# Kernel tuning notes

Measured on AMD Instinct MI355X. Metric: run time of the kernel, lower is better.

## Reference

```python
import jax, jax.numpy as jnp
import numpy as np

SPATIAL = ((100, 100), (50, 50), (25, 25), (13, 13))
STARTS = [0]
for _h, _w in SPATIAL[:-1]:
    STARTS.append(STARTS[-1] + _h * _w)
L_TOTAL = sum(h * w for h, w in SPATIAL)  # 13294
D, DFFN, NL, NH, NP = 256, 1024, 4, 8, 4
DH = D // NH
EPS = 1e-5


def _ln(x, g, b):
    mu = x.mean(-1, keepdims=True)
    var = ((x - mu) ** 2).mean(-1, keepdims=True)
    return (x - mu) * jax.lax.rsqrt(var + EPS) * g + b


def _bilinear(v_l, x, y, H, W):
    # v_l: [B,NH,H*W,DH]; x,y: [B,NH,Q*NP] pixel coords (grid_sample align_corners=False, zero padding)
    x0f = jnp.floor(x); y0f = jnp.floor(y)
    lx, ly = x - x0f, y - y0f
    x0 = x0f.astype(jnp.int32); y0 = y0f.astype(jnp.int32)
    acc = 0.0
    for dx, dy, w in ((0, 0, (1 - lx) * (1 - ly)), (1, 0, lx * (1 - ly)),
                      (0, 1, (1 - lx) * ly), (1, 1, lx * ly)):
        xi, yi = x0 + dx, y0 + dy
        valid = (xi >= 0) & (xi < W) & (yi >= 0) & (yi < H)
        idx = jnp.clip(yi, 0, H - 1) * W + jnp.clip(xi, 0, W - 1)
        g = jnp.take_along_axis(v_l, idx[..., None], axis=2)  # [B,NH,Q*NP,DH]
        acc = acc + g * (w * valid.astype(w.dtype))[..., None]
    return acc


def _msdeform(query, value_in, ref, norm_wh, Woff, boff, Wattn, battn, Wval, bval, Wout, bout):
    B, Q, _ = query.shape
    v = (value_in @ Wval + bval).reshape(B, L_TOTAL, NH, DH)
    off = (query @ Woff + boff).reshape(B, Q, NH, NL, NP, 2)
    aw = (query @ Wattn + battn).reshape(B, Q, NH, NL * NP)
    aw = jax.nn.softmax(aw, axis=-1).reshape(B, Q, NH, NL, NP)
    # normalized sampling locations in [0,1]: ref + offset / (W,H)
    loc = ref[:, :, None, :, None, :] + off / norm_wh[None, None, None, :, None, :]
    out = 0.0
    for l, (H, W) in enumerate(SPATIAL):
        s = STARTS[l]
        v_l = v[:, s:s + H * W].transpose(0, 2, 1, 3)          # [B,NH,HW,DH]
        loc_l = loc[:, :, :, l].transpose(0, 2, 1, 3, 4)       # [B,NH,Q,NP,2]
        x = (loc_l[..., 0] * W - 0.5).reshape(B, NH, Q * NP)
        y = (loc_l[..., 1] * H - 0.5).reshape(B, NH, Q * NP)
        samp = _bilinear(v_l, x, y, H, W).reshape(B, NH, Q, NP, DH)
        w_l = aw[:, :, :, l].transpose(0, 2, 1, 3)             # [B,NH,Q,NP]
        out = out + (samp * w_l[..., None]).sum(3)             # [B,NH,Q,DH]
    out = out.transpose(0, 2, 1, 3).reshape(B, Q, D)
    return out @ Wout + bout


def setup_inputs() -> dict:
    key = jax.random.key(0)
    ks = jax.random.split(key, 12)
    B = 4
    s = 0.02
    return {
        "src": jax.random.normal(ks[0], (B, L_TOTAL, D), jnp.float32),
        "pos": jax.random.normal(ks[1], (B, L_TOTAL, D), jnp.float32),
        "reference_points": jax.random.uniform(ks[2], (B, L_TOTAL, NL, 2), jnp.float32),
        "spatial_shapes": jnp.array(SPATIAL, jnp.int32),
        "level_start_index": jnp.array(STARTS, jnp.int32),
        "W_off": jax.random.normal(ks[3], (D, NH * NL * NP * 2), jnp.float32) * 0.01,
        "b_off": jax.random.normal(ks[4], (NH * NL * NP * 2,), jnp.float32) * 0.5,
        "W_attn": jax.random.normal(ks[5], (D, NH * NL * NP), jnp.float32) * s,
        "b_attn": jnp.zeros((NH * NL * NP,), jnp.float32),
        "W_val": jax.random.normal(ks[6], (D, D), jnp.float32) * s,
        "b_val": jnp.zeros((D,), jnp.float32),
        "W_out": jax.random.normal(ks[7], (D, D), jnp.float32) * s,
        "b_out": jnp.zeros((D,), jnp.float32),
        "ln_sa_g": jnp.ones((D,), jnp.float32),
        "ln_sa_b": jnp.zeros((D,), jnp.float32),
        "W1": jax.random.normal(ks[8], (D, DFFN), jnp.float32) * s,
        "b1": jnp.zeros((DFFN,), jnp.float32),
        "W2": jax.random.normal(ks[9], (DFFN, D), jnp.float32) * s,
        "b2": jnp.zeros((D,), jnp.float32),
        "ln_ff_g": jnp.ones((D,), jnp.float32),
        "ln_ff_b": jnp.zeros((D,), jnp.float32),
    }


def reference(src, pos, reference_points, spatial_shapes, level_start_index,
              W_off, b_off, W_attn, b_attn, W_val, b_val, W_out, b_out,
              ln_sa_g, ln_sa_b, W1, b1, W2, b2, ln_ff_g, ln_ff_b):
    # offset normalizer is (W, H) per level
    norm_wh = jnp.stack([spatial_shapes[:, 1], spatial_shapes[:, 0]], -1).astype(src.dtype)
    q = src + pos  # with_pos_embed
    sa = _msdeform(q, src, reference_points, norm_wh,
                   W_off, b_off, W_attn, b_attn, W_val, b_val, W_out, b_out)
    x = _ln(sa + src, ln_sa_g, ln_sa_b)          # dropout = identity (eval)
    y = jnp.maximum(x @ W1 + b1, 0.0) @ W2 + b2  # relu FFN
    return _ln(y + x, ln_ff_g, ln_ff_b)
```

## Files before the change

kernel.cpp:

```cpp
#include <hip/hip_runtime.h>
#include <hip/hip_bf16.h>

typedef __hip_bfloat16 bf16;
typedef short bf16x8 __attribute__((ext_vector_type(8)));
typedef float f32x4  __attribute__((ext_vector_type(4)));

#define ROWS 53176
#define LTOT 13294

__device__ __forceinline__ float b2f(bf16 v) { return __bfloat162float(v); }

__device__ __forceinline__ void gl2lds16(const void* g, void* l) {
    __builtin_amdgcn_global_load_lds(
        (const __attribute__((address_space(1))) unsigned*)g,
        (__attribute__((address_space(3))) unsigned*)l, 16, 0, 0);
}

template<bool RELU>
__global__ __launch_bounds__(256, 2)
void gemm_bs_n(const bf16* __restrict__ A, const bf16* __restrict__ Bt,
               const float* __restrict__ bias, bf16* __restrict__ C,
               int M, int N)
{
    __shared__ __align__(16) char Bsb[65536];
    const int tid  = threadIdx.x;
    const int wave = tid >> 6, lane = tid & 63;
    const int l15 = lane & 15, quad = lane >> 4;
    const int swz = (lane & 7) << 4;
    const int m0 = blockIdx.y * 256, n0 = blockIdx.x * 128;

    const char* Btb = (const char*)(Bt + (size_t)n0 * 256);
#pragma unroll
    for (int it = 0; it < 16; ++it) {
        int c = it * 256 + tid;
        int srcoff = (c * 16) ^ (((c >> 5) & 7) << 4);
        gl2lds16(Btb + srcoff, Bsb + (it * 256 + wave * 64) * 16);
    }

    const bf16* aptr[4];
#pragma unroll
    for (int i = 0; i < 4; ++i) {
        int r = m0 + wave * 64 + i * 16 + l15;
        if (r > M - 1) r = M - 1;
        aptr[i] = A + (size_t)r * 256;
    }

    f32x4 acc[4][8];
#pragma unroll
    for (int i = 0; i < 4; ++i)
#pragma unroll
        for (int j = 0; j < 8; ++j) acc[i][j] = (f32x4){0.f, 0.f, 0.f, 0.f};

    __syncthreads();

#pragma unroll
    for (int kc = 0; kc < 8; ++kc) {
        bf16x8 af[4], bfr[8];
#pragma unroll
        for (int i = 0; i < 4; ++i)
            af[i] = *(const bf16x8*)(aptr[i] + kc * 32 + quad * 8);
#pragma unroll
        for (int j = 0; j < 8; ++j) {
            int boff = ((j * 16 + l15) * 512 + kc * 64 + quad * 16) ^ swz;
            bfr[j] = *(const bf16x8*)&Bsb[boff];
        }
#pragma unroll
        for (int i = 0; i < 4; ++i)
#pragma unroll
            for (int j = 0; j < 8; ++j)
                acc[i][j] = __builtin_amdgcn_mfma_f32_16x16x32_bf16(bfr[j], af[i], acc[i][j], 0, 0, 0);
    }

    float4 b4[8];
#pragma unroll
    for (int j = 0; j < 8; ++j)
        b4[j] = *(const float4*)&bias[n0 + j * 16 + quad * 4];

#pragma unroll
    for (int i = 0; i < 4; ++i) {
        int gm = m0 + wave * 64 + i * 16 + l15;
        if (gm >= M) continue;
#pragma unroll
        for (int j = 0; j < 8; ++j) {
            int gn = n0 + j * 16 + quad * 4;
            union { bf16 h[4]; uint2 u2; } pk;
#pragma unroll
            for (int r = 0; r < 4; ++r) {
                float v = acc[i][j][r] + ((const float*)&b4[j])[r];
                if (RELU) v = fmaxf(v, 0.f);
                pk.h[r] = __float2bfloat16(v);
            }
            *(uint2*)&C[(size_t)gm * N + gn] = pk.u2;
        }
    }
}

template<typename OT, int K>
__global__ __launch_bounds__(256, 2)
void gemm_bs_ln(const bf16* __restrict__ A, const bf16* __restrict__ Bt,
                const float* __restrict__ bias, const bf16* __restrict__ res,
                OT* __restrict__ C, const float* __restrict__ gam,
                const float* __restrict__ bet, int M)
{
    __shared__ __align__(16) char Bsb[65536];
    const int tid  = threadIdx.x;
    const int wave = tid >> 6, lane = tid & 63;
    const int l15 = lane & 15, quad = lane >> 4;
    const int swz = (lane & 7) << 4;
    const int m0 = blockIdx.x * 128;

    const bf16* aptr[2];
#pragma unroll
    for (int i = 0; i < 2; ++i) {
        int r = m0 + wave * 32 + i * 16 + l15;
        if (r > M - 1) r = M - 1;
        aptr[i] = A + (size_t)r * K;
    }

    f32x4 acc[2][16];
#pragma unroll
    for (int i = 0; i < 2; ++i)
#pragma unroll
        for (int j = 0; j < 16; ++j) acc[i][j] = (f32x4){0.f, 0.f, 0.f, 0.f};

    for (int kc = 0; kc < K / 128; ++kc) {
#pragma unroll
        for (int it = 0; it < 16; ++it) {
            int c = it * 256 + tid;
            int row = c >> 4, col = c & 15;
            size_t srcoff = (size_t)row * (K * 2) + kc * 256
                          + ((col * 16) ^ ((row & 7) << 4));
            gl2lds16((const char*)Bt + srcoff, Bsb + (it * 256 + wave * 64) * 16);
        }
        __syncthreads();
#pragma unroll
        for (int t = 0; t < 4; ++t) {
            bf16x8 af[2], bfr[16];
#pragma unroll
            for (int i = 0; i < 2; ++i)
                af[i] = *(const bf16x8*)(aptr[i] + kc * 128 + t * 32 + quad * 8);
#pragma unroll
            for (int j = 0; j < 16; ++j) {
                int boff = ((j * 16 + l15) * 256 + t * 64 + quad * 16) ^ swz;
                bfr[j] = *(const bf16x8*)&Bsb[boff];
            }
#pragma unroll
            for (int i = 0; i < 2; ++i)
#pragma unroll
                for (int j = 0; j < 16; ++j)
                    acc[i][j] = __builtin_amdgcn_mfma_f32_16x16x32_bf16(bfr[j], af[i], acc[i][j], 0, 0, 0);
        }
        __syncthreads();
    }

#pragma unroll
    for (int i = 0; i < 2; ++i) {
        int gm = m0 + wave * 32 + i * 16 + l15;
        bool valid = gm < M;
        float lsum = 0.f, lsq = 0.f;
#pragma unroll
        for (int j = 0; j < 16; ++j) {
            int gn = j * 16 + quad * 4;
            float4 b4 = *(const float4*)&bias[gn];
            float r4[4] = {0.f, 0.f, 0.f, 0.f};
            if (valid) {
                uint2 ru = *(const uint2*)&res[(size_t)gm * 256 + gn];
                const bf16* rh = (const bf16*)&ru;
#pragma unroll
                for (int r = 0; r < 4; ++r) r4[r] = b2f(rh[r]);
            }
#pragma unroll
            for (int r = 0; r < 4; ++r) {
                float v = acc[i][j][r] + ((const float*)&b4)[r] + r4[r];
                acc[i][j][r] = v;
                lsum += v;
                lsq  += v * v;
            }
        }
#pragma unroll
        for (int mask = 16; mask <= 32; mask <<= 1) {
            lsum += __shfl_xor(lsum, mask);
            lsq  += __shfl_xor(lsq, mask);
        }
        if (!valid) continue;
        float mean = lsum * (1.f / 256.f);
        float var  = lsq * (1.f / 256.f) - mean * mean;
        float rstd = rsqrtf(fmaxf(var, 0.f) + 1e-5f);
#pragma unroll
        for (int j = 0; j < 16; ++j) {
            int gn = j * 16 + quad * 4;
            float4 g4  = *(const float4*)&gam[gn];
            float4 be4 = *(const float4*)&bet[gn];
            if constexpr (sizeof(OT) == 2) {
                union { bf16 h[4]; uint2 u2; } pk;
#pragma unroll
                for (int r = 0; r < 4; ++r)
                    pk.h[r] = __float2bfloat16((acc[i][j][r] - mean) * rstd *
                              ((const float*)&g4)[r] + ((const float*)&be4)[r]);
                *(uint2*)&((bf16*)C)[(size_t)gm * 256 + gn] = pk.u2;
            } else {
                float4 o;
#pragma unroll
                for (int r = 0; r < 4; ++r)
                    ((float*)&o)[r] = (acc[i][j][r] - mean) * rstd *
                              ((const float*)&g4)[r] + ((const float*)&be4)[r];
                *(float4*)&((float*)C)[(size_t)gm * 256 + gn] = o;
            }
        }
    }
}

__global__ void cast_qs_kernel(const float* __restrict__ s, const float* __restrict__ p,
                               bf16* __restrict__ sb, bf16* __restrict__ qb, int n4)
{
    int i = blockIdx.x * 256 + threadIdx.x;
    if (i >= n4) return;
    float4 sv = ((const float4*)s)[i];
    float4 pv = ((const float4*)p)[i];
    union { bf16 h[4]; uint2 u; } a, b;
    a.h[0] = __float2bfloat16(sv.x); a.h[1] = __float2bfloat16(sv.y);
    a.h[2] = __float2bfloat16(sv.z); a.h[3] = __float2bfloat16(sv.w);
    b.h[0] = __float2bfloat16(sv.x + pv.x); b.h[1] = __float2bfloat16(sv.y + pv.y);
    b.h[2] = __float2bfloat16(sv.z + pv.z); b.h[3] = __float2bfloat16(sv.w + pv.w);
    ((uint2*)sb)[i] = a.u;
    ((uint2*)qb)[i] = b.u;
}

__global__ void wcast_all(const float* __restrict__ Wval, const float* __restrict__ Woff,
                          const float* __restrict__ Wattn, const float* __restrict__ Wout,
                          const float* __restrict__ W1, const float* __restrict__ W2,
                          const float* __restrict__ boff, const float* __restrict__ battn,
                          bf16* __restrict__ Wval_t, bf16* __restrict__ Wcat_t,
                          bf16* __restrict__ Wout_t, bf16* __restrict__ W1_t,
                          bf16* __restrict__ W2_t, float* __restrict__ bcat)
{
    int e = blockIdx.x * 256 + threadIdx.x;
    if (e < 384) bcat[e] = (e < 256) ? boff[e] : battn[e - 256];
    if (e < 65536) {
        int n = e >> 8, k = e & 255;
        Wval_t[e] = __float2bfloat16(Wval[k * 256 + n]);
    } else if (e < 163840) {
        int i = e - 65536; int n = i >> 8, k = i & 255;
        float w = (n < 256) ? Woff[k * 256 + n] : Wattn[k * 128 + (n - 256)];
        Wcat_t[i] = __float2bfloat16(w);
    } else if (e < 229376) {
        int i = e - 163840; int n = i >> 8, k = i & 255;
        Wout_t[i] = __float2bfloat16(Wout[k * 256 + n]);
    } else if (e < 491520) {
        int i = e - 229376; int n = i >> 8, k = i & 255;
        W1_t[i] = __float2bfloat16(W1[k * 1024 + n]);
    } else if (e < 753664) {
        int i = e - 491520; int n = i >> 10, k = i & 1023;
        W2_t[i] = __float2bfloat16(W2[k * 256 + n]);
    }
}

__global__ __launch_bounds__(256)
void sample_kernel(const bf16* __restrict__ v, const bf16* __restrict__ ocat,
                   const float* __restrict__ ref, bf16* __restrict__ samp)
{
    __shared__ int4 tab[16][33];
    const int tid = threadIdx.x;
    const int grp = tid >> 4, lane = tid & 15;
    const int gidx = blockIdx.x * 16 + grp;
    const int h = gidx & 7, bq = gidx >> 3, b = bq / LTOT;

    {
        const int p = lane, l = p >> 2, pp = p & 3;
        const int W = (l == 0) ? 100 : (l == 1) ? 50 : (l == 2) ? 25 : 13;
        const int S = (l == 0) ? 0 : (l == 1) ? 10000 : (l == 2) ? 12500 : 13125;
        const float fW = (float)W;
        float rx = ref[(size_t)bq * 8 + l * 2 + 0];
        float ry = ref[(size_t)bq * 8 + l * 2 + 1];
        const bf16* ob = ocat + (size_t)bq * 384;
        float ox = b2f(ob[h * 32 + l * 8 + pp * 2 + 0]);
        float oy = b2f(ob[h * 32 + l * 8 + pp * 2 + 1]);
        float lg = b2f(ob[256 + h * 16 + p]);
        float m = lg;
#pragma unroll
        for (int mask = 1; mask <= 8; mask <<= 1) m = fmaxf(m, __shfl_xor(m, mask));
        float ev = __expf(lg - m);
        float s = ev;
#pragma unroll
        for (int mask = 1; mask <= 8; mask <<= 1) s += __shfl_xor(s, mask);
        float wgt = ev / s;

        float x = fmaf(rx, fW, ox - 0.5f);
        float y = fmaf(ry, fW, oy - 0.5f);
        float x0f = floorf(x), y0f = floorf(y);
        float lx = x - x0f, ly = y - y0f;
        int x0 = (int)x0f, y0 = (int)y0f;
        float tw[4] = {(1.f - lx) * (1.f - ly), lx * (1.f - ly),
                       (1.f - lx) * ly,         lx * ly};
        const int base = (b * LTOT + S) * 512 + h * 64;
        int  o[4]; float w[4];
#pragma unroll
        for (int t = 0; t < 4; ++t) {
            int xi = x0 + (t & 1), yi = y0 + (t >> 1);
            bool ok = (xi >= 0) & (xi < W) & (yi >= 0) & (yi < W);
            o[t] = ok ? base + (yi * W + xi) * 512 : 0;
            w[t] = ok ? wgt * tw[t] : 0.f;
        }
        tab[grp][p * 2 + 0] = make_int4(o[0], __float_as_int(w[0]), o[1], __float_as_int(w[1]));
        tab[grp][p * 2 + 1] = make_int4(o[2], __float_as_int(w[2]), o[3], __float_as_int(w[3]));
    }
    __syncthreads();

    const int lofs = lane * 4;
    const char* vc = (const char*)v;
    float a0 = 0.f, a1 = 0.f;
#pragma unroll 4
    for (int e2 = 0; e2 < 32; ++e2) {
        int4 q = tab[grp][e2];
        unsigned u0 = *(const unsigned*)(vc + (size_t)(unsigned)(q.x + lofs));
        unsigned u1 = *(const unsigned*)(vc + (size_t)(unsigned)(q.z + lofs));
        float w0 = __int_as_float(q.y), w1 = __int_as_float(q.w);
        a0 += w0 * __uint_as_float(u0 << 16);
        a1 += w0 * __uint_as_float(u0);
        a0 += w1 * __uint_as_float(u1 << 16);
        a1 += w1 * __uint_as_float(u1);
    }
    union { struct { bf16 a, b; } h2; unsigned u; } r;
    r.h2.a = __float2bfloat16(a0);
    r.h2.b = __float2bfloat16(a1);
    *(unsigned*)((char*)samp + (size_t)gidx * 64 + lane * 4) = r.u;
}

extern "C" void kernel_launch(void* const* d_in, const int* in_sizes, int n_in,
                              void* d_out, int out_size, void* d_ws, size_t ws_size,
                              hipStream_t stream)
{
    const float* src     = (const float*)d_in[0];
    const float* pos     = (const float*)d_in[1];
    const float* ref     = (const float*)d_in[2];
    const float* W_off   = (const float*)d_in[5];
    const float* b_off   = (const float*)d_in[6];
    const float* W_attn  = (const float*)d_in[7];
    const float* b_attn  = (const float*)d_in[8];
    const float* W_val   = (const float*)d_in[9];
    const float* b_val   = (const float*)d_in[10];
    const float* W_out   = (const float*)d_in[11];
    const float* b_out   = (const float*)d_in[12];
    const float* ln_sa_g = (const float*)d_in[13];
    const float* ln_sa_b = (const float*)d_in[14];
    const float* W1      = (const float*)d_in[15];
    const float* b1      = (const float*)d_in[16];
    const float* W2      = (const float*)d_in[17];
    const float* b2      = (const float*)d_in[18];
    const float* ln_ff_g = (const float*)d_in[19];
    const float* ln_ff_b = (const float*)d_in[20];

    char* ws = (char*)d_ws;
    bf16* sb     = (bf16*)(ws);
    bf16* qb     = (bf16*)(ws + 27226112);
    bf16* samp   = (bf16*)(ws + 27226112);
    bf16* vbuf   = (bf16*)(ws + 54452224);
    bf16* ocat   = (bf16*)(ws + 81678336);
    bf16* xb16   = (bf16*)(ws + 122517504);
    bf16* hbuf   = (bf16*)(ws);
    bf16* Wval_t = (bf16*)(ws + 149743616);
    bf16* Wcat_t = (bf16*)(ws + 149874688);
    float* bcat  = (float*)(ws + 150071296);
    bf16* Wout_t = (bf16*)(ws + 150072832);
    bf16* W1_t   = (bf16*)(ws + 150203904);
    bf16* W2_t   = (bf16*)(ws + 150728192);
    float* outf  = (float*)d_out;

    dim3 blk(256);

    cast_qs_kernel<<<dim3((ROWS * 64 + 255) / 256), blk, 0, stream>>>(src, pos, sb, qb, ROWS * 64);
    wcast_all<<<dim3(2944), blk, 0, stream>>>(W_val, W_off, W_attn, W_out, W1, W2,
                                              b_off, b_attn,
                                              Wval_t, Wcat_t, Wout_t, W1_t, W2_t, bcat);

    gemm_bs_n<false><<<dim3(2, 208), blk, 0, stream>>>(sb, Wval_t, b_val, vbuf, ROWS, 256);
    gemm_bs_n<false><<<dim3(3, 208), blk, 0, stream>>>(qb, Wcat_t, bcat, ocat, ROWS, 384);
    sample_kernel<<<dim3(ROWS * 8 / 16), blk, 0, stream>>>(vbuf, ocat, ref, samp);
    gemm_bs_ln<bf16, 256><<<dim3(416), blk, 0, stream>>>(
        samp, Wout_t, b_out, sb, xb16, ln_sa_g, ln_sa_b, ROWS);
    gemm_bs_n<true><<<dim3(8, 208), blk, 0, stream>>>(xb16, W1_t, b1, hbuf, ROWS, 1024);
    gemm_bs_ln<float, 1024><<<dim3(416), blk, 0, stream>>>(
        hbuf, W2_t, b2, xb16, outf, ln_ff_g, ln_ff_b, ROWS);
}
```

Before: 541.6 us.

## Shrink GEMM tiles for more blocks and split LayerNorm GEMM columns across waves

The value and offset/attention projections now use 64-column tiles with half the LDS and a higher occupancy bound, which doubles their grid size. The LayerNorm-fused GEMMs use 64-row tiles where each wave handles 128 columns, with row statistics combined through LDS atomics, and the grid grows from 416 to 831 blocks. The aim is to fill more of the CUs and overlap more waves per CU. The cost is reloading more B data per block and adding an extra sync plus shared atomics.

```diff
diff --git a/kernel.cpp b/kernel.cpp
--- a/kernel.cpp
+++ b/kernel.cpp
@@ -16,25 +16,25 @@
         (__attribute__((address_space(3))) unsigned*)l, 16, 0, 0);
 }
 
-template<bool RELU>
-__global__ __launch_bounds__(256, 2)
+template<bool RELU, int COLS>
+__global__ __launch_bounds__(256, COLS == 64 ? 4 : 2)
 void gemm_bs_n(const bf16* __restrict__ A, const bf16* __restrict__ Bt,
                const float* __restrict__ bias, bf16* __restrict__ C,
                int M, int N)
 {
-    __shared__ __align__(16) char Bsb[65536];
+    constexpr int NJ = COLS / 16;
+    __shared__ __align__(16) char Bsb[COLS * 512];
     const int tid  = threadIdx.x;
     const int wave = tid >> 6, lane = tid & 63;
     const int l15 = lane & 15, quad = lane >> 4;
-    const int swz = (lane & 7) << 4;
-    const int m0 = blockIdx.y * 256, n0 = blockIdx.x * 128;
-
-    const char* Btb = (const char*)(Bt + (size_t)n0 * 256);
-#pragma unroll
-    for (int it = 0; it < 16; ++it) {
+    const int m0 = blockIdx.y * 256, n0 = blockIdx.x * COLS;
+
+#pragma unroll
+    for (int it = 0; it < COLS / 8; ++it) {
         int c = it * 256 + tid;
-        int srcoff = (c * 16) ^ (((c >> 5) & 7) << 4);
-        gl2lds16(Btb + srcoff, Bsb + (it * 256 + wave * 64) * 16);
+        int rowN = c >> 5, kb = (c & 31) * 16;
+        size_t srcoff = (size_t)(n0 + rowN) * 512 + (kb ^ ((rowN & 7) << 4));
+        gl2lds16((const char*)Bt + srcoff, Bsb + c * 16);
     }
 
     const bf16* aptr[4];
@@ -45,35 +45,36 @@
         aptr[i] = A + (size_t)r * 256;
     }
 
-    f32x4 acc[4][8];
+    f32x4 acc[4][NJ];
 #pragma unroll
     for (int i = 0; i < 4; ++i)
 #pragma unroll
-        for (int j = 0; j < 8; ++j) acc[i][j] = (f32x4){0.f, 0.f, 0.f, 0.f};
+        for (int j = 0; j < NJ; ++j) acc[i][j] = (f32x4){0.f, 0.f, 0.f, 0.f};
 
     __syncthreads();
 
 #pragma unroll
     for (int kc = 0; kc < 8; ++kc) {
-        bf16x8 af[4], bfr[8];
+        bf16x8 af[4], bfr[NJ];
 #pragma unroll
         for (int i = 0; i < 4; ++i)
             af[i] = *(const bf16x8*)(aptr[i] + kc * 32 + quad * 8);
 #pragma unroll
-        for (int j = 0; j < 8; ++j) {
-            int boff = ((j * 16 + l15) * 512 + kc * 64 + quad * 16) ^ swz;
+        for (int j = 0; j < NJ; ++j) {
+            int rowN = j * 16 + l15;
+            int boff = rowN * 512 + ((kc * 64 + quad * 16) ^ ((rowN & 7) << 4));
             bfr[j] = *(const bf16x8*)&Bsb[boff];
         }
 #pragma unroll
         for (int i = 0; i < 4; ++i)
 #pragma unroll
-            for (int j = 0; j < 8; ++j)
+            for (int j = 0; j < NJ; ++j)
                 acc[i][j] = __builtin_amdgcn_mfma_f32_16x16x32_bf16(bfr[j], af[i], acc[i][j], 0, 0, 0);
     }
 
-    float4 b4[8];
-#pragma unroll
-    for (int j = 0; j < 8; ++j)
+    float4 b4[NJ];
+#pragma unroll
+    for (int j = 0; j < NJ; ++j)
         b4[j] = *(const float4*)&bias[n0 + j * 16 + quad * 4];
 
 #pragma unroll
@@ -81,7 +82,7 @@
         int gm = m0 + wave * 64 + i * 16 + l15;
         if (gm >= M) continue;
 #pragma unroll
-        for (int j = 0; j < 8; ++j) {
+        for (int j = 0; j < NJ; ++j) {
             int gn = n0 + j * 16 + quad * 4;
             union { bf16 h[4]; uint2 u2; } pk;
 #pragma unroll
@@ -96,71 +97,76 @@
 }
 
 template<typename OT, int K>
-__global__ __launch_bounds__(256, 2)
-void gemm_bs_ln(const bf16* __restrict__ A, const bf16* __restrict__ Bt,
-                const float* __restrict__ bias, const bf16* __restrict__ res,
-                OT* __restrict__ C, const float* __restrict__ gam,
-                const float* __restrict__ bet, int M)
-{
-    __shared__ __align__(16) char Bsb[65536];
+__global__ __launch_bounds__(256, 4)
+void gemm_ln2(const bf16* __restrict__ A, const bf16* __restrict__ Bt,
+              const float* __restrict__ bias, const bf16* __restrict__ res,
+              OT* __restrict__ C, const float* __restrict__ gam,
+              const float* __restrict__ bet, int M)
+{
+    __shared__ __align__(16) char Bsb[32768];
+    __shared__ float rsum[64], rsq[64];
     const int tid  = threadIdx.x;
     const int wave = tid >> 6, lane = tid & 63;
     const int l15 = lane & 15, quad = lane >> 4;
-    const int swz = (lane & 7) << 4;
-    const int m0 = blockIdx.x * 128;
+    const int m0 = blockIdx.x * 64;
+    const int wr = (wave >> 1) * 32;
+    const int wc = (wave & 1) * 128;
+    if (tid < 64) { rsum[tid] = 0.f; rsq[tid] = 0.f; }
 
     const bf16* aptr[2];
 #pragma unroll
     for (int i = 0; i < 2; ++i) {
-        int r = m0 + wave * 32 + i * 16 + l15;
+        int r = m0 + wr + i * 16 + l15;
         if (r > M - 1) r = M - 1;
         aptr[i] = A + (size_t)r * K;
     }
 
-    f32x4 acc[2][16];
+    f32x4 acc[2][8];
 #pragma unroll
     for (int i = 0; i < 2; ++i)
 #pragma unroll
-        for (int j = 0; j < 16; ++j) acc[i][j] = (f32x4){0.f, 0.f, 0.f, 0.f};
-
-    for (int kc = 0; kc < K / 128; ++kc) {
-#pragma unroll
-        for (int it = 0; it < 16; ++it) {
+        for (int j = 0; j < 8; ++j) acc[i][j] = (f32x4){0.f, 0.f, 0.f, 0.f};
+
+    for (int kc = 0; kc < K / 64; ++kc) {
+#pragma unroll
+        for (int it = 0; it < 8; ++it) {
             int c = it * 256 + tid;
-            int row = c >> 4, col = c & 15;
-            size_t srcoff = (size_t)row * (K * 2) + kc * 256
-                          + ((col * 16) ^ ((row & 7) << 4));
-            gl2lds16((const char*)Bt + srcoff, Bsb + (it * 256 + wave * 64) * 16);
+            int rowN = c >> 3, kb = (c & 7) * 16;
+            size_t srcoff = (size_t)rowN * (K * 2) + kc * 128
+                          + (kb ^ ((rowN & 7) << 4));
+            gl2lds16((const char*)Bt + srcoff, Bsb + c * 16);
         }
         __syncthreads();
 #pragma unroll
-        for (int t = 0; t < 4; ++t) {
-            bf16x8 af[2], bfr[16];
+        for (int t = 0; t < 2; ++t) {
+            bf16x8 af[2], bfr[8];
 #pragma unroll
             for (int i = 0; i < 2; ++i)
-                af[i] = *(const bf16x8*)(aptr[i] + kc * 128 + t * 32 + quad * 8);
-#pragma unroll
-            for (int j = 0; j < 16; ++j) {
-                int boff = ((j * 16 + l15) * 256 + t * 64 + quad * 16) ^ swz;
+                af[i] = *(const bf16x8*)(aptr[i] + kc * 64 + t * 32 + quad * 8);
+#pragma unroll
+            for (int j = 0; j < 8; ++j) {
+                int rowN = wc + j * 16 + l15;
+                int boff = rowN * 128 + ((t * 64 + quad * 16) ^ ((rowN & 7) << 4));
                 bfr[j] = *(const bf16x8*)&Bsb[boff];
             }
 #pragma unroll
             for (int i = 0; i < 2; ++i)
 #pragma unroll
-                for (int j = 0; j < 16; ++j)
+                for (int j = 0; j < 8; ++j)
                     acc[i][j] = __builtin_amdgcn_mfma_f32_16x16x32_bf16(bfr[j], af[i], acc[i][j], 0, 0, 0);
         }
         __syncthreads();
     }
 
+    float lsum[2], lsq[2];
 #pragma unroll
     for (int i = 0; i < 2; ++i) {
-        int gm = m0 + wave * 32 + i * 16 + l15;
+        int gm = m0 + wr + i * 16 + l15;
         bool valid = gm < M;
-        float lsum = 0.f, lsq = 0.f;
-#pragma unroll
-        for (int j = 0; j < 16; ++j) {
-            int gn = j * 16 + quad * 4;
+        lsum[i] = 0.f; lsq[i] = 0.f;
+#pragma unroll
+        for (int j = 0; j < 8; ++j) {
+            int gn = wc + j * 16 + quad * 4;
             float4 b4 = *(const float4*)&bias[gn];
             float r4[4] = {0.f, 0.f, 0.f, 0.f};
             if (valid) {
@@ -173,22 +179,36 @@
             for (int r = 0; r < 4; ++r) {
                 float v = acc[i][j][r] + ((const float*)&b4)[r] + r4[r];
                 acc[i][j][r] = v;
-                lsum += v;
-                lsq  += v * v;
+                lsum[i] += v;
+                lsq[i]  += v * v;
             }
         }
 #pragma unroll
         for (int mask = 16; mask <= 32; mask <<= 1) {
-            lsum += __shfl_xor(lsum, mask);
-            lsq  += __shfl_xor(lsq, mask);
-        }
-        if (!valid) continue;
-        float mean = lsum * (1.f / 256.f);
-        float var  = lsq * (1.f / 256.f) - mean * mean;
+            lsum[i] += __shfl_xor(lsum[i], mask);
+            lsq[i]  += __shfl_xor(lsq[i], mask);
+        }
+    }
+    if (quad == 0) {
+#pragma unroll
+        for (int i = 0; i < 2; ++i) {
+            atomicAdd(&rsum[wr + i * 16 + l15], lsum[i]);
+            atomicAdd(&rsq [wr + i * 16 + l15], lsq[i]);
+        }
+    }
+    __syncthreads();
+
+#pragma unroll
+    for (int i = 0; i < 2; ++i) {
+        int lr = wr + i * 16 + l15;
+        int gm = m0 + lr;
+        if (gm >= M) continue;
+        float mean = rsum[lr] * (1.f / 256.f);
+        float var  = rsq[lr] * (1.f / 256.f) - mean * mean;
         float rstd = rsqrtf(fmaxf(var, 0.f) + 1e-5f);
 #pragma unroll
-        for (int j = 0; j < 16; ++j) {
-            int gn = j * 16 + quad * 4;
+        for (int j = 0; j < 8; ++j) {
+            int gn = wc + j * 16 + quad * 4;
             float4 g4  = *(const float4*)&gam[gn];
             float4 be4 = *(const float4*)&bet[gn];
             if constexpr (sizeof(OT) == 2) {
@@ -373,12 +393,12 @@
                                               b_off, b_attn,
                                               Wval_t, Wcat_t, Wout_t, W1_t, W2_t, bcat);
 
-    gemm_bs_n<false><<<dim3(2, 208), blk, 0, stream>>>(sb, Wval_t, b_val, vbuf, ROWS, 256);
-    gemm_bs_n<false><<<dim3(3, 208), blk, 0, stream>>>(qb, Wcat_t, bcat, ocat, ROWS, 384);
+    gemm_bs_n<false, 64><<<dim3(4, 208), blk, 0, stream>>>(sb, Wval_t, b_val, vbuf, ROWS, 256);
+    gemm_bs_n<false, 64><<<dim3(6, 208), blk, 0, stream>>>(qb, Wcat_t, bcat, ocat, ROWS, 384);
     sample_kernel<<<dim3(ROWS * 8 / 16), blk, 0, stream>>>(vbuf, ocat, ref, samp);
-    gemm_bs_ln<bf16, 256><<<dim3(416), blk, 0, stream>>>(
+    gemm_ln2<bf16, 256><<<dim3(831), blk, 0, stream>>>(
         samp, Wout_t, b_out, sb, xb16, ln_sa_g, ln_sa_b, ROWS);
-    gemm_bs_n<true><<<dim3(8, 208), blk, 0, stream>>>(xb16, W1_t, b1, hbuf, ROWS, 1024);
-    gemm_bs_ln<float, 1024><<<dim3(416), blk, 0, stream>>>(
+    gemm_bs_n<true, 128><<<dim3(8, 208), blk, 0, stream>>>(xb16, W1_t, b1, hbuf, ROWS, 1024);
+    gemm_ln2<float, 1024><<<dim3(831), blk, 0, stream>>>(
         hbuf, W2_t, b2, xb16, outf, ln_ff_g, ln_ff_b, ROWS);
 }
```

Measured after the change: 544.4 us. No clear change (+0.5%).
